# Kernel optimization log

Measured on AMD Instinct MI355X. Metric: run time of the kernel, lower is better.

Reference implementation:

```python
import jax, jax.numpy as jnp
import numpy as np
import math

B, T, D = 2, 2048, 1024
NH = 16
HD = D // NH


def setup_inputs() -> dict:
    key = jax.random.key(0)
    k1, k2, k3 = jax.random.split(key, 3)
    scale = 0.02
    x = jax.random.normal(k1, (B, T, D), dtype=jnp.float32)
    Wqkv = jax.random.normal(k2, (D, 3 * D), dtype=jnp.float32) * scale
    bqkv = jnp.zeros((3 * D,), dtype=jnp.float32)
    Wproj = jax.random.normal(k3, (D, D), dtype=jnp.float32) * scale
    bproj = jnp.zeros((D,), dtype=jnp.float32)
    return {"x": x, "Wqkv": Wqkv, "bqkv": bqkv, "Wproj": Wproj, "bproj": bproj}


def reference(x, Wqkv, bqkv, Wproj, bproj):
    b, t, c = x.shape
    qkv = x @ Wqkv + bqkv                      # [B,T,3D]
    q, k, v = jnp.split(qkv, 3, axis=2)
    # [B,T,NH,HD] -> [B,NH,T,HD]
    q = q.reshape(b, t, NH, HD).transpose(0, 2, 1, 3)
    k = k.reshape(b, t, NH, HD).transpose(0, 2, 1, 3)
    v = v.reshape(b, t, NH, HD).transpose(0, 2, 1, 3)
    att = jnp.einsum('bhqd,bhkd->bhqk', q, k) / math.sqrt(HD)  # [B,NH,T,T]
    causal = jnp.tril(jnp.ones((t, t), dtype=bool))
    att = jnp.where(causal, att, -jnp.inf)
    att = jax.nn.softmax(att, axis=-1)
    y = jnp.einsum('bhqk,bhkd->bhqd', att, v)  # [B,NH,T,HD]
    y = y.transpose(0, 2, 1, 3).reshape(b, t, c)
    return y @ Wproj + bproj
```

## Files before the change

kernel.cpp:

```cpp
#include <hip/hip_runtime.h>
#include <hip/hip_bf16.h>

#define B_   2
#define T_   2048
#define D_   1024
#define NH_  16
#define HD_  64
#define MROWS (B_*T_)
#define HEADELEMS (B_*NH_*T_*HD_)

#define QSCALE 0.180336880f

typedef unsigned short u16;
typedef unsigned int   u32;

typedef float f32x4  __attribute__((ext_vector_type(4)));
typedef short bf16x8 __attribute__((ext_vector_type(8)));

#define GLP(g, l) __builtin_amdgcn_global_load_lds(                         \
    (const __attribute__((address_space(1))) void*)(g),                     \
    (__attribute__((address_space(3))) void*)(l), 16, 0, 0)

struct Fc { static constexpr bool value = false; };
struct Tc { static constexpr bool value = true;  };

__device__ __forceinline__ u16 f2bf(float f) {
    u32 x = __float_as_uint(f);
    u32 r = (x + 0x7fffu + ((x >> 16) & 1u)) >> 16;
    return (u16)r;
}
__device__ __forceinline__ u32 pkbf2(float a, float b) {
    __hip_bfloat162 h = __float22bfloat162_rn(make_float2(a, b));
    union { __hip_bfloat162 h2; u32 u; } cv; cv.h2 = h; return cv.u;
}

__device__ __forceinline__ void transpose_tile(const float* in, u16* out,
                                               int K, int N, int bx, int by,
                                               int t, float (*Ts)[65])
{
    const int n0 = bx * 64;
    const int k0 = by * 64;
    #pragma unroll
    for (int pass = 0; pass < 4; pass++) {
        const int r = pass * 16 + (t >> 4);
        const int c = (t & 15) * 4;
        float4 v = *(const float4*)(in + (size_t)(k0 + r) * N + n0 + c);
        Ts[r][c] = v.x; Ts[r][c+1] = v.y; Ts[r][c+2] = v.z; Ts[r][c+3] = v.w;
    }
    __syncthreads();
    #pragma unroll
    for (int pass = 0; pass < 2; pass++) {
        const int nn = pass * 32 + (t >> 3);
        const int kk = (t & 7) * 8;
        u16 o[8];
        #pragma unroll
        for (int j = 0; j < 8; j++) o[j] = f2bf(Ts[kk + j][nn]);
        *(uint4*)(out + (size_t)(n0 + nn) * K + k0 + kk) = *(const uint4*)o;
    }
}

__global__ __launch_bounds__(256)
void prep_kernel(const float* __restrict__ x, const float* __restrict__ Wqkv,
                 const float* __restrict__ Wproj, u16* __restrict__ xb,
                 u16* __restrict__ WqkvT, u16* __restrict__ WprojT)
{
    __shared__ float Ts[64][65];
    const int bid = blockIdx.x;
    const int t   = threadIdx.x;
    if (bid < 4096) {
        int i = bid * 256 + t;
        float4 v = ((const float4*)x)[i];
        ushort4 o;
        o.x = f2bf(v.x); o.y = f2bf(v.y); o.z = f2bf(v.z); o.w = f2bf(v.w);
        ((ushort4*)xb)[i] = o;
    } else if (bid < 4096 + 768) {
        int tb = bid - 4096;
        transpose_tile(Wqkv, WqkvT, D_, 3*D_, tb % 48, tb / 48, t, Ts);
    } else {
        int tb = bid - 4864;
        transpose_tile(Wproj, WprojT, D_, D_, tb % 16, tb / 16, t, Ts);
    }
}

__global__ __launch_bounds__(256)
void transpose_conv_kernel(const float* __restrict__ in, u16* __restrict__ out,
                           int K, int N)
{
    __shared__ float Ts[64][65];
    transpose_tile(in, out, K, N, blockIdx.x, blockIdx.y, threadIdx.x, Ts);
}

template <int MODE>
__global__ __launch_bounds__(256)
void gemm_mfma(const u16* __restrict__ A, const u16* __restrict__ BT,
               const float* __restrict__ bias, void* __restrict__ outv,
               int M, int N, int K)
{
    __shared__ u16 As[2][128][32];
    __shared__ u16 Bs[2][128][32];

    const int t    = threadIdx.x;
    const int wave = t >> 6;
    const int lane = t & 63;
    const int l16  = lane & 15;
    const int quad = lane >> 4;

    const int m0 = blockIdx.y * 128;
    const int n0 = blockIdx.x * 128;
    const int mb = (wave >> 1) * 64;
    const int nb = (wave & 1) * 64;

    const int r0a  = wave * 16;
    const int r0b  = 64 + wave * 16;
    const int lr_a = r0a + (lane >> 2);
    const int lr_b = r0b + (lane >> 2);
    const int sega = (((lane & 3) ^ ((lr_a >> 1) & 3))) * 8;
    const int segb = (((lane & 3) ^ ((lr_b >> 1) & 3))) * 8;

    const u16* gA0 = A  + (size_t)(m0 + lr_a) * K + sega;
    const u16* gA1 = A  + (size_t)(m0 + lr_b) * K + segb;
    const u16* gB0 = BT + (size_t)(n0 + lr_a) * K + sega;
    const u16* gB1 = BT + (size_t)(n0 + lr_b) * K + segb;

    const int fragoff = (quad ^ ((l16 >> 1) & 3)) * 8;

    f32x4 acc[4][4];
    #pragma unroll
    for (int i = 0; i < 4; i++)
        #pragma unroll
        for (int j = 0; j < 4; j++) acc[i][j] = (f32x4){0,0,0,0};

    GLP(gA0, &As[0][r0a][0]);
    GLP(gA1, &As[0][r0b][0]);
    GLP(gB0, &Bs[0][r0a][0]);
    GLP(gB1, &Bs[0][r0b][0]);
    __syncthreads();

    const int nk = K >> 5;
    for (int kt = 0; kt < nk; ++kt) {
        const int cur = kt & 1;
        if (kt + 1 < nk) {
            const int nxt = cur ^ 1;
            const int kn  = (kt + 1) << 5;
            GLP(gA0 + kn, &As[nxt][r0a][0]);
            GLP(gA1 + kn, &As[nxt][r0b][0]);
            GLP(gB0 + kn, &Bs[nxt][r0a][0]);
            GLP(gB1 + kn, &Bs[nxt][r0b][0]);
        }

        bf16x8 af[4], bfr[4];
        #pragma unroll
        for (int i = 0; i < 4; i++)
            af[i] = *(const bf16x8*)&As[cur][mb + i*16 + l16][fragoff];
        #pragma unroll
        for (int j = 0; j < 4; j++)
            bfr[j] = *(const bf16x8*)&Bs[cur][nb + j*16 + l16][fragoff];

        #pragma unroll
        for (int i = 0; i < 4; i++)
            #pragma unroll
            for (int j = 0; j < 4; j++)
                acc[i][j] = __builtin_amdgcn_mfma_f32_16x16x32_bf16(
                    af[i], bfr[j], acc[i][j], 0, 0, 0);

        __syncthreads();
    }

    if (MODE == 0) {
        #pragma unroll
        for (int j = 0; j < 4; j++) {
            const int n = n0 + nb + j*16 + l16;
            const float bv = bias[n];
            #pragma unroll
            for (int i = 0; i < 4; i++) {
                #pragma unroll
                for (int r = 0; r < 4; r++) {
                    const int m = m0 + mb + i*16 + quad*4 + r;
                    ((float*)outv)[(size_t)m * N + n] = acc[i][j][r] + bv;
                }
            }
        }
    } else {
        const int sec = n0 >> 10;
        const int b   = m0 >> 11;
        const int tb  = m0 & 2047;
        if (sec < 2) {
            const float qs = (sec == 0) ? QSCALE : 1.f;
            #pragma unroll
            for (int j = 0; j < 4; j++) {
                const int n  = n0 + nb + j*16 + l16;
                const float bv = bias[n];
                const int dd = n & 1023;
                const int h  = dd >> 6;
                const int hd = dd & 63;
                u16* op = (u16*)outv + (size_t)sec * HEADELEMS
                        + ((size_t)(b*NH_ + h)) * T_ * HD_ + hd;
                #pragma unroll
                for (int i = 0; i < 4; i++) {
                    #pragma unroll
                    for (int r = 0; r < 4; r++) {
                        const int tt = tb + mb + i*16 + quad*4 + r;
                        op[(size_t)tt * HD_] = f2bf((acc[i][j][r] + bv) * qs);
                    }
                }
            }
        } else {
            #pragma unroll
            for (int j = 0; j < 4; j++) {
                const int n  = n0 + nb + j*16 + l16;
                const float bv = bias[n];
                const int dd = n & 1023;
                const int h  = dd >> 6;
                const int hd = dd & 63;
                u16* vp = (u16*)outv + (size_t)2 * HEADELEMS
                        + ((size_t)(b*NH_ + h)) * T_ * HD_
                        + (size_t)hd * T_ + tb + mb;
                #pragma unroll
                for (int i = 0; i < 4; i++) {
                    u16 o[4];
                    #pragma unroll
                    for (int r = 0; r < 4; r++) o[r] = f2bf(acc[i][j][r] + bv);
                    *(uint2*)(vp + i*16 + quad*4) = *(const uint2*)o;
                }
            }
        }
    }
}

__global__ __launch_bounds__(256)
void attn_mfma_kernel(const u16* __restrict__ Q, const u16* __restrict__ K,
                      const u16* __restrict__ VT, u16* __restrict__ y1)
{
    __shared__ u16 Ks[2][64][72];
    __shared__ u16 Vs[2][64][72];

    const int t    = threadIdx.x;
    const int wave = t >> 6;
    const int lane = t & 63;
    const int l16  = lane & 15;
    const int quad = lane >> 4;

    const int hb = blockIdx.x;
    const int yy = blockIdx.y;
    const int a  = yy & 7, g = yy >> 3;
    const int qt = (g == 0) ? 31 - a : (g == 1) ? 16 + a
                 : (g == 2) ? 15 - a : a;
    const int b  = hb >> 4;
    const int h  = hb & 15;
    const size_t base = (size_t)hb * T_ * HD_;

    const int qw0 = qt * 64 + wave * 16;

    bf16x8 qf[2];
    {
        const u16* qp = Q + base + (size_t)(qw0 + l16) * HD_ + quad * 8;
        qf[0] = *(const bf16x8*)(qp);
        qf[1] = *(const bf16x8*)(qp + 32);
    }

    bf16x8 onesf;
    #pragma unroll
    for (int i = 0; i < 8; i++) onesf[i] = (short)0x3F80;

    f32x4 o[4];
    #pragma unroll
    for (int d = 0; d < 4; d++) o[d] = (f32x4){0,0,0,0};
    f32x4 accl = (f32x4){0,0,0,0};

    const int nsteps = qt + 1;

    const int srow = t >> 3;
    const int scol = (t & 7) * 8;

    const int srcA  = l16 + ((quad & 1) << 5);
    const int srcB  = srcA + 16;
    const bool selhi = (quad >> 1) != 0;

    uint4 kr0, kr1, vr0, vr1;
    {
        const u16* kp = K + base + (size_t)srow * HD_ + scol;
        kr0 = *(const uint4*)kp;
        kr1 = *(const uint4*)(kp + 32 * HD_);
        const u16* vp = VT + base + (size_t)srow * T_ + scol;
        vr0 = *(const uint4*)vp;
        vr1 = *(const uint4*)(vp + 32 * T_);
        *(uint4*)&Ks[0][srow][scol]      = kr0;
        *(uint4*)&Ks[0][srow + 32][scol] = kr1;
        *(uint4*)&Vs[0][srow][scol]      = vr0;
        *(uint4*)&Vs[0][srow + 32][scol] = vr1;
    }
    __syncthreads();

    auto compute_tile = [&](int cur, int k0, auto mc) {
        constexpr bool MASKED = decltype(mc)::value;
        f32x4 st[4];
        #pragma unroll
        for (int j = 0; j < 4; j++) {
            bf16x8 kf0 = *(const bf16x8*)&Ks[cur][j*16 + l16][quad * 8];
            bf16x8 kf1 = *(const bf16x8*)&Ks[cur][j*16 + l16][32 + quad * 8];
            f32x4 z = {0,0,0,0};
            z = __builtin_amdgcn_mfma_f32_16x16x32_bf16(kf0, qf[0], z, 0, 0, 0);
            st[j] = __builtin_amdgcn_mfma_f32_16x16x32_bf16(kf1, qf[1], z, 0, 0, 0);
        }

        u32 p01[4], p23[4];
        const int qi = qw0 + l16;
        #pragma unroll
        for (int j = 0; j < 4; j++) {
            const int kb = k0 + j*16 + quad*4;
            float e0 = __builtin_amdgcn_exp2f(st[j][0]);
            float e1 = __builtin_amdgcn_exp2f(st[j][1]);
            float e2 = __builtin_amdgcn_exp2f(st[j][2]);
            float e3 = __builtin_amdgcn_exp2f(st[j][3]);
            if (MASKED) {
                if (kb + 0 > qi) e0 = 0.f;
                if (kb + 1 > qi) e1 = 0.f;
                if (kb + 2 > qi) e2 = 0.f;
                if (kb + 3 > qi) e3 = 0.f;
            }
            p01[j] = pkbf2(e0, e1);
            p23[j] = pkbf2(e2, e3);
        }

        bf16x8 pf[2];
        #pragma unroll
        for (int c = 0; c < 2; c++) {
            u32 t0, t1, r01, r23, r45, r67;
            t0 = (u32)__shfl((int)p01[2*c],   srcA);
            t1 = (u32)__shfl((int)p01[2*c+1], srcA);
            r01 = selhi ? t1 : t0;
            t0 = (u32)__shfl((int)p23[2*c],   srcA);
            t1 = (u32)__shfl((int)p23[2*c+1], srcA);
            r23 = selhi ? t1 : t0;
            t0 = (u32)__shfl((int)p01[2*c],   srcB);
            t1 = (u32)__shfl((int)p01[2*c+1], srcB);
            r45 = selhi ? t1 : t0;
            t0 = (u32)__shfl((int)p23[2*c],   srcB);
            t1 = (u32)__shfl((int)p23[2*c+1], srcB);
            r67 = selhi ? t1 : t0;
            union { u32 u[4]; bf16x8 v; } pk;
            pk.u[0] = r01; pk.u[1] = r23; pk.u[2] = r45; pk.u[3] = r67;
            pf[c] = pk.v;
        }
        accl = __builtin_amdgcn_mfma_f32_16x16x32_bf16(pf[0], onesf, accl, 0, 0, 0);
        accl = __builtin_amdgcn_mfma_f32_16x16x32_bf16(pf[1], onesf, accl, 0, 0, 0);
        #pragma unroll
        for (int d = 0; d < 4; d++) {
            bf16x8 v0 = *(const bf16x8*)&Vs[cur][d*16 + l16][quad * 8];
            bf16x8 v1 = *(const bf16x8*)&Vs[cur][d*16 + l16][32 + quad * 8];
            o[d] = __builtin_amdgcn_mfma_f32_16x16x32_bf16(pf[0], v0, o[d], 0, 0, 0);
            o[d] = __builtin_amdgcn_mfma_f32_16x16x32_bf16(pf[1], v1, o[d], 0, 0, 0);
        }
    };

    for (int kt = 0; kt < nsteps; kt++) {
        const int cur = kt & 1;
        const int k0  = kt * 64;
        const bool have_next = (kt + 1 < nsteps);

        if (have_next) {
            const u16* kp = K + base + (size_t)(k0 + 64 + srow) * HD_ + scol;
            kr0 = *(const uint4*)kp;
            kr1 = *(const uint4*)(kp + 32 * HD_);
            const u16* vp = VT + base + (size_t)srow * T_ + k0 + 64 + scol;
            vr0 = *(const uint4*)vp;
            vr1 = *(const uint4*)(vp + 32 * T_);
        }

        if (kt < qt) compute_tile(cur, k0, Fc{});
        else         compute_tile(cur, k0, Tc{});

        if (have_next) {
            const int nxt = cur ^ 1;
            *(uint4*)&Ks[nxt][srow][scol]      = kr0;
            *(uint4*)&Ks[nxt][srow + 32][scol] = kr1;
            *(uint4*)&Vs[nxt][srow][scol]      = vr0;
            *(uint4*)&Vs[nxt][srow + 32][scol] = vr1;
            __syncthreads();
        }
    }

    #pragma unroll
    for (int r = 0; r < 4; r++) {
        const float inv = 1.f / accl[r];
        const int qi = qw0 + quad*4 + r;
        u16* yp = y1 + ((size_t)(b * T_ + qi)) * D_ + h * HD_ + l16;
        yp[0]  = f2bf(o[0][r] * inv);
        yp[16] = f2bf(o[1][r] * inv);
        yp[32] = f2bf(o[2][r] * inv);
        yp[48] = f2bf(o[3][r] * inv);
    }
}

extern "C" void kernel_launch(void* const* d_in, const int* in_sizes, int n_in,
                              void* d_out, int out_size, void* d_ws, size_t ws_size,
                              hipStream_t stream)
{
    const float* x     = (const float*)d_in[0];
    const float* Wqkv  = (const float*)d_in[1];
    const float* bqkv  = (const float*)d_in[2];
    const float* Wproj = (const float*)d_in[3];
    const float* bproj = (const float*)d_in[4];

    u16* scratch = (u16*)d_out;
    u16* xb      = scratch;
    u16* WqkvT   = scratch + (size_t)MROWS * D_;

    const size_t Y1E = (size_t)MROWS * D_;
    const size_t WPE = (size_t)D_ * D_;

    u16* qkv = (u16*)d_ws;
    u16* Qp  = qkv;
    u16* Kp  = qkv + (size_t)HEADELEMS;
    u16* Vtp = qkv + (size_t)2 * HEADELEMS;

    const bool huge = ws_size >= ((size_t)3 * HEADELEMS + Y1E + WPE) * 2;
    const bool big  = ws_size >= ((size_t)3 * HEADELEMS + Y1E) * 2;

    u16* y1b    = big ? qkv + (size_t)3 * HEADELEMS : scratch;
    u16* y1g    = big ? y1b : Vtp;
    u16* WprojT = huge ? qkv + (size_t)3 * HEADELEMS + Y1E : Kp;

    prep_kernel<<<huge ? 5120 : 4864, 256, 0, stream>>>(
        x, Wqkv, Wproj, xb, WqkvT, WprojT);

    gemm_mfma<1><<<dim3(3*D_/128, MROWS/128), 256, 0, stream>>>(
        xb, WqkvT, bqkv, (void*)qkv, MROWS, 3*D_, D_);

    attn_mfma_kernel<<<dim3(NH_*B_, T_/64), 256, 0, stream>>>(Qp, Kp, Vtp, y1b);

    if (!huge)
        transpose_conv_kernel<<<dim3(D_/64, D_/64), 256, 0, stream>>>(
            Wproj, WprojT, D_, D_);

    if (!big)
        (void)hipMemcpyAsync(y1g, y1b, Y1E * sizeof(u16),
                             hipMemcpyDeviceToDevice, stream);

    gemm_mfma<0><<<dim3(D_/128, MROWS/128), 256, 0, stream>>>(
        y1g, WprojT, bproj, d_out, MROWS, D_, D_);
}
```

Before: 200.2 us.

## Shrink GEMM tiles to 64x128 with two waves, drop double buffering, add setprio in attention

```diff
diff --git a/kernel.cpp b/kernel.cpp
--- a/kernel.cpp
+++ b/kernel.cpp
@@ -91,13 +91,13 @@
 }
 
 template <int MODE>
-__global__ __launch_bounds__(256)
+__global__ __launch_bounds__(128)
 void gemm_mfma(const u16* __restrict__ A, const u16* __restrict__ BT,
                const float* __restrict__ bias, void* __restrict__ outv,
                int M, int N, int K)
 {
-    __shared__ u16 As[2][128][32];
-    __shared__ u16 Bs[2][128][32];
+    __shared__ u16 As[64][32];
+    __shared__ u16 Bs[128][32];
 
     const int t    = threadIdx.x;
     const int wave = t >> 6;
@@ -105,22 +105,23 @@
     const int l16  = lane & 15;
     const int quad = lane >> 4;
 
-    const int m0 = blockIdx.y * 128;
+    const int m0 = blockIdx.y * 64;
     const int n0 = blockIdx.x * 128;
-    const int mb = (wave >> 1) * 64;
-    const int nb = (wave & 1) * 64;
-
-    const int r0a  = wave * 16;
-    const int r0b  = 64 + wave * 16;
-    const int lr_a = r0a + (lane >> 2);
-    const int lr_b = r0b + (lane >> 2);
-    const int sega = (((lane & 3) ^ ((lr_a >> 1) & 3))) * 8;
-    const int segb = (((lane & 3) ^ ((lr_b >> 1) & 3))) * 8;
-
-    const u16* gA0 = A  + (size_t)(m0 + lr_a) * K + sega;
-    const u16* gA1 = A  + (size_t)(m0 + lr_b) * K + segb;
-    const u16* gB0 = BT + (size_t)(n0 + lr_a) * K + sega;
-    const u16* gB1 = BT + (size_t)(n0 + lr_b) * K + segb;
+    const int nb = wave * 64;
+
+    const int lrow = lane >> 2;
+    const int seg  = (((lane & 3) ^ ((lane >> 3) & 3))) * 8;
+
+    const int ra0 = wave * 32;
+    const int ra1 = wave * 32 + 16;
+    const int rb0 = wave * 64;
+
+    const u16* gA0 = A  + (size_t)(m0 + ra0 + lrow) * K + seg;
+    const u16* gA1 = A  + (size_t)(m0 + ra1 + lrow) * K + seg;
+    const u16* gB0 = BT + (size_t)(n0 + rb0      + lrow) * K + seg;
+    const u16* gB1 = BT + (size_t)(n0 + rb0 + 16 + lrow) * K + seg;
+    const u16* gB2 = BT + (size_t)(n0 + rb0 + 32 + lrow) * K + seg;
+    const u16* gB3 = BT + (size_t)(n0 + rb0 + 48 + lrow) * K + seg;
 
     const int fragoff = (quad ^ ((l16 >> 1) & 3)) * 8;
 
@@ -130,31 +131,23 @@
         #pragma unroll
         for (int j = 0; j < 4; j++) acc[i][j] = (f32x4){0,0,0,0};
 
-    GLP(gA0, &As[0][r0a][0]);
-    GLP(gA1, &As[0][r0b][0]);
-    GLP(gB0, &Bs[0][r0a][0]);
-    GLP(gB1, &Bs[0][r0b][0]);
-    __syncthreads();
-
-    const int nk = K >> 5;
-    for (int kt = 0; kt < nk; ++kt) {
-        const int cur = kt & 1;
-        if (kt + 1 < nk) {
-            const int nxt = cur ^ 1;
-            const int kn  = (kt + 1) << 5;
-            GLP(gA0 + kn, &As[nxt][r0a][0]);
-            GLP(gA1 + kn, &As[nxt][r0b][0]);
-            GLP(gB0 + kn, &Bs[nxt][r0a][0]);
-            GLP(gB1 + kn, &Bs[nxt][r0b][0]);
-        }
+    for (int k0 = 0; k0 < K; k0 += 32) {
+        __syncthreads();
+        GLP(gA0 + k0, &As[ra0][0]);
+        GLP(gA1 + k0, &As[ra1][0]);
+        GLP(gB0 + k0, &Bs[rb0][0]);
+        GLP(gB1 + k0, &Bs[rb0 + 16][0]);
+        GLP(gB2 + k0, &Bs[rb0 + 32][0]);
+        GLP(gB3 + k0, &Bs[rb0 + 48][0]);
+        __syncthreads();
 
         bf16x8 af[4], bfr[4];
         #pragma unroll
         for (int i = 0; i < 4; i++)
-            af[i] = *(const bf16x8*)&As[cur][mb + i*16 + l16][fragoff];
+            af[i] = *(const bf16x8*)&As[i*16 + l16][fragoff];
         #pragma unroll
         for (int j = 0; j < 4; j++)
-            bfr[j] = *(const bf16x8*)&Bs[cur][nb + j*16 + l16][fragoff];
+            bfr[j] = *(const bf16x8*)&Bs[nb + j*16 + l16][fragoff];
 
         #pragma unroll
         for (int i = 0; i < 4; i++)
@@ -162,8 +155,6 @@
             for (int j = 0; j < 4; j++)
                 acc[i][j] = __builtin_amdgcn_mfma_f32_16x16x32_bf16(
                     af[i], bfr[j], acc[i][j], 0, 0, 0);
-
-        __syncthreads();
     }
 
     if (MODE == 0) {
@@ -175,7 +166,7 @@
             for (int i = 0; i < 4; i++) {
                 #pragma unroll
                 for (int r = 0; r < 4; r++) {
-                    const int m = m0 + mb + i*16 + quad*4 + r;
+                    const int m = m0 + i*16 + quad*4 + r;
                     ((float*)outv)[(size_t)m * N + n] = acc[i][j][r] + bv;
                 }
             }
@@ -199,7 +190,7 @@
                 for (int i = 0; i < 4; i++) {
                     #pragma unroll
                     for (int r = 0; r < 4; r++) {
-                        const int tt = tb + mb + i*16 + quad*4 + r;
+                        const int tt = tb + i*16 + quad*4 + r;
                         op[(size_t)tt * HD_] = f2bf((acc[i][j][r] + bv) * qs);
                     }
                 }
@@ -214,7 +205,7 @@
                 const int hd = dd & 63;
                 u16* vp = (u16*)outv + (size_t)2 * HEADELEMS
                         + ((size_t)(b*NH_ + h)) * T_ * HD_
-                        + (size_t)hd * T_ + tb + mb;
+                        + (size_t)hd * T_ + tb;
                 #pragma unroll
                 for (int i = 0; i < 4; i++) {
                     u16 o[4];
@@ -294,6 +285,7 @@
     auto compute_tile = [&](int cur, int k0, auto mc) {
         constexpr bool MASKED = decltype(mc)::value;
         f32x4 st[4];
+        __builtin_amdgcn_s_setprio(1);
         #pragma unroll
         for (int j = 0; j < 4; j++) {
             bf16x8 kf0 = *(const bf16x8*)&Ks[cur][j*16 + l16][quad * 8];
@@ -302,6 +294,7 @@
             z = __builtin_amdgcn_mfma_f32_16x16x32_bf16(kf0, qf[0], z, 0, 0, 0);
             st[j] = __builtin_amdgcn_mfma_f32_16x16x32_bf16(kf1, qf[1], z, 0, 0, 0);
         }
+        __builtin_amdgcn_s_setprio(0);
 
         u32 p01[4], p23[4];
         const int qi = qw0 + l16;
@@ -342,6 +335,7 @@
             pk.u[0] = r01; pk.u[1] = r23; pk.u[2] = r45; pk.u[3] = r67;
             pf[c] = pk.v;
         }
+        __builtin_amdgcn_s_setprio(1);
         accl = __builtin_amdgcn_mfma_f32_16x16x32_bf16(pf[0], onesf, accl, 0, 0, 0);
         accl = __builtin_amdgcn_mfma_f32_16x16x32_bf16(pf[1], onesf, accl, 0, 0, 0);
         #pragma unroll
@@ -351,6 +345,7 @@
             o[d] = __builtin_amdgcn_mfma_f32_16x16x32_bf16(pf[0], v0, o[d], 0, 0, 0);
             o[d] = __builtin_amdgcn_mfma_f32_16x16x32_bf16(pf[1], v1, o[d], 0, 0, 0);
         }
+        __builtin_amdgcn_s_setprio(0);
     };
 
     for (int kt = 0; kt < nsteps; kt++) {
@@ -424,7 +419,7 @@
     prep_kernel<<<huge ? 5120 : 4864, 256, 0, stream>>>(
         x, Wqkv, Wproj, xb, WqkvT, WprojT);
 
-    gemm_mfma<1><<<dim3(3*D_/128, MROWS/128), 256, 0, stream>>>(
+    gemm_mfma<1><<<dim3(3*D_/128, MROWS/64), 128, 0, stream>>>(
         xb, WqkvT, bqkv, (void*)qkv, MROWS, 3*D_, D_);
 
     attn_mfma_kernel<<<dim3(NH_*B_, T_/64), 256, 0, stream>>>(Qp, Kp, Vtp, y1b);
@@ -437,6 +432,6 @@
         (void)hipMemcpyAsync(y1g, y1b, Y1E * sizeof(u16),
                              hipMemcpyDeviceToDevice, stream);
 
-    gemm_mfma<0><<<dim3(D_/128, MROWS/128), 256, 0, stream>>>(
+    gemm_mfma<0><<<dim3(D_/128, MROWS/64), 128, 0, stream>>>(
         y1g, WprojT, bproj, d_out, MROWS, D_, D_);
 }
```

New measurement: 208.3 us. 1.04x slower.

## Use single-buffered 64-wide K tiles in GEMM and raise MFMA wave priority in attention

Applied to the files above, without the earlier changes.

```diff
diff --git a/kernel.cpp b/kernel.cpp
--- a/kernel.cpp
+++ b/kernel.cpp
@@ -96,8 +96,8 @@
                const float* __restrict__ bias, void* __restrict__ outv,
                int M, int N, int K)
 {
-    __shared__ u16 As[2][128][32];
-    __shared__ u16 Bs[2][128][32];
+    __shared__ u16 As[128][64];
+    __shared__ u16 Bs[128][64];
 
     const int t    = threadIdx.x;
     const int wave = t >> 6;
@@ -110,19 +110,14 @@
     const int mb = (wave >> 1) * 64;
     const int nb = (wave & 1) * 64;
 
-    const int r0a  = wave * 16;
-    const int r0b  = 64 + wave * 16;
-    const int lr_a = r0a + (lane >> 2);
-    const int lr_b = r0b + (lane >> 2);
-    const int sega = (((lane & 3) ^ ((lr_a >> 1) & 3))) * 8;
-    const int segb = (((lane & 3) ^ ((lr_b >> 1) & 3))) * 8;
-
-    const u16* gA0 = A  + (size_t)(m0 + lr_a) * K + sega;
-    const u16* gA1 = A  + (size_t)(m0 + lr_b) * K + segb;
-    const u16* gB0 = BT + (size_t)(n0 + lr_a) * K + sega;
-    const u16* gB1 = BT + (size_t)(n0 + lr_b) * K + segb;
-
-    const int fragoff = (quad ^ ((l16 >> 1) & 3)) * 8;
+    const int srow = lane >> 3;
+    const int sseg = ((lane & 7) ^ srow) * 8;
+
+    const int rw = wave * 32;
+    const u16* gA = A  + (size_t)(m0 + rw + srow) * K + sseg;
+    const u16* gB = BT + (size_t)(n0 + rw + srow) * K + sseg;
+
+    const int fragcol = (quad ^ (l16 & 7)) * 8;
 
     f32x4 acc[4][4];
     #pragma unroll
@@ -130,40 +125,36 @@
         #pragma unroll
         for (int j = 0; j < 4; j++) acc[i][j] = (f32x4){0,0,0,0};
 
-    GLP(gA0, &As[0][r0a][0]);
-    GLP(gA1, &As[0][r0b][0]);
-    GLP(gB0, &Bs[0][r0a][0]);
-    GLP(gB1, &Bs[0][r0b][0]);
-    __syncthreads();
-
-    const int nk = K >> 5;
-    for (int kt = 0; kt < nk; ++kt) {
-        const int cur = kt & 1;
-        if (kt + 1 < nk) {
-            const int nxt = cur ^ 1;
-            const int kn  = (kt + 1) << 5;
-            GLP(gA0 + kn, &As[nxt][r0a][0]);
-            GLP(gA1 + kn, &As[nxt][r0b][0]);
-            GLP(gB0 + kn, &Bs[nxt][r0a][0]);
-            GLP(gB1 + kn, &Bs[nxt][r0b][0]);
-        }
-
-        bf16x8 af[4], bfr[4];
-        #pragma unroll
-        for (int i = 0; i < 4; i++)
-            af[i] = *(const bf16x8*)&As[cur][mb + i*16 + l16][fragoff];
-        #pragma unroll
-        for (int j = 0; j < 4; j++)
-            bfr[j] = *(const bf16x8*)&Bs[cur][nb + j*16 + l16][fragoff];
-
-        #pragma unroll
-        for (int i = 0; i < 4; i++)
+    for (int k0 = 0; k0 < K; k0 += 64) {
+        __syncthreads();
+        GLP(gA + k0,            &As[rw     ][0]);
+        GLP(gA + k0 +  8*K,     &As[rw +  8][0]);
+        GLP(gA + k0 + 16*K,     &As[rw + 16][0]);
+        GLP(gA + k0 + 24*K,     &As[rw + 24][0]);
+        GLP(gB + k0,            &Bs[rw     ][0]);
+        GLP(gB + k0 +  8*K,     &Bs[rw +  8][0]);
+        GLP(gB + k0 + 16*K,     &Bs[rw + 16][0]);
+        GLP(gB + k0 + 24*K,     &Bs[rw + 24][0]);
+        __syncthreads();
+
+        #pragma unroll
+        for (int kk = 0; kk < 2; kk++) {
+            const int fc = fragcol ^ (kk << 5);
+            bf16x8 af[4], bfr[4];
+            #pragma unroll
+            for (int i = 0; i < 4; i++)
+                af[i] = *(const bf16x8*)&As[mb + i*16 + l16][fc];
             #pragma unroll
             for (int j = 0; j < 4; j++)
-                acc[i][j] = __builtin_amdgcn_mfma_f32_16x16x32_bf16(
-                    af[i], bfr[j], acc[i][j], 0, 0, 0);
-
-        __syncthreads();
+                bfr[j] = *(const bf16x8*)&Bs[nb + j*16 + l16][fc];
+
+            #pragma unroll
+            for (int i = 0; i < 4; i++)
+                #pragma unroll
+                for (int j = 0; j < 4; j++)
+                    acc[i][j] = __builtin_amdgcn_mfma_f32_16x16x32_bf16(
+                        af[i], bfr[j], acc[i][j], 0, 0, 0);
+        }
     }
 
     if (MODE == 0) {
@@ -294,6 +285,7 @@
     auto compute_tile = [&](int cur, int k0, auto mc) {
         constexpr bool MASKED = decltype(mc)::value;
         f32x4 st[4];
+        __builtin_amdgcn_s_setprio(1);
         #pragma unroll
         for (int j = 0; j < 4; j++) {
             bf16x8 kf0 = *(const bf16x8*)&Ks[cur][j*16 + l16][quad * 8];
@@ -302,6 +294,7 @@
             z = __builtin_amdgcn_mfma_f32_16x16x32_bf16(kf0, qf[0], z, 0, 0, 0);
             st[j] = __builtin_amdgcn_mfma_f32_16x16x32_bf16(kf1, qf[1], z, 0, 0, 0);
         }
+        __builtin_amdgcn_s_setprio(0);
 
         u32 p01[4], p23[4];
         const int qi = qw0 + l16;
@@ -342,6 +335,7 @@
             pk.u[0] = r01; pk.u[1] = r23; pk.u[2] = r45; pk.u[3] = r67;
             pf[c] = pk.v;
         }
+        __builtin_amdgcn_s_setprio(1);
         accl = __builtin_amdgcn_mfma_f32_16x16x32_bf16(pf[0], onesf, accl, 0, 0, 0);
         accl = __builtin_amdgcn_mfma_f32_16x16x32_bf16(pf[1], onesf, accl, 0, 0, 0);
         #pragma unroll
@@ -351,6 +345,7 @@
             o[d] = __builtin_amdgcn_mfma_f32_16x16x32_bf16(pf[0], v0, o[d], 0, 0, 0);
             o[d] = __builtin_amdgcn_mfma_f32_16x16x32_bf16(pf[1], v1, o[d], 0, 0, 0);
         }
+        __builtin_amdgcn_s_setprio(0);
     };
 
     for (int kt = 0; kt < nsteps; kt++) {
```

New measurement: 196.0 us. 2.1% less time.
